# Kernel optimization log

Measured on AMD Instinct MI355X. Metric: run time of the kernel, lower is better.

The kernel has to match this reference:

```python
import jax, jax.numpy as jnp
import numpy as np

NUM_TAGS = 16
PAD_ID, START_ID, STOP_ID = 0, 14, 15
NEG = -10000.0
B, T, K = 1024, 512, NUM_TAGS


def setup_inputs() -> dict:
    key = jax.random.key(0)
    kh, kt, ky, kl = jax.random.split(key, 4)
    # transition matrix trans[to, from], with constraints from crf.__init__
    trans = jax.random.normal(kt, (K, K), jnp.float32)
    trans = (trans.at[START_ID, :].set(NEG)
                  .at[:, STOP_ID].set(NEG)
                  .at[:, PAD_ID].set(NEG)
                  .at[PAD_ID, :].set(NEG)
                  .at[PAD_ID, STOP_ID].set(0.0)
                  .at[PAD_ID, PAD_ID].set(0.0))
    # variable-length prefix mask (gt(0) on token ids in the original)
    lengths = jax.random.randint(kl, (B,), 1, T + 1)
    mask = (jnp.arange(T)[None, :] < lengths[:, None]).astype(jnp.float32)
    # gold tags: real tags in 1..13 on valid positions, PAD elsewhere
    y = 1 + jax.random.randint(ky, (B, T), 0, 13)
    y = jnp.where(mask > 0, y, PAD_ID).astype(jnp.int64)
    # emissions (output of fc in Net.forward)
    h = jax.random.normal(kh, (B, T, K), jnp.float32)
    return {"h": h, "y": y, "mask": mask, "trans": trans}


def _crf_forward_score(h, mask, trans):
    # partition function via log-sum-exp recurrence (crf.forward)
    alpha0 = jnp.full((h.shape[0], K), NEG, h.dtype).at[:, START_ID].set(0.0)

    def step(alpha, xs):
        emit_t, mask_t = xs  # [B,K], [B]
        # score.unsqueeze(1) + emit.unsqueeze(2) + trans -> [B, new, prev]
        s = alpha[:, None, :] + emit_t[:, :, None] + trans[None, :, :]
        new = jax.nn.logsumexp(s, axis=-1)  # [B,K]
        m = mask_t[:, None]
        return new * m + alpha * (1.0 - m), None

    alpha, _ = jax.lax.scan(step, alpha0,
                            (jnp.swapaxes(h, 0, 1), jnp.swapaxes(mask, 0, 1)))
    return jax.nn.logsumexp(alpha + trans[STOP_ID][None, :], axis=-1)  # [B]


def _crf_gold_score(h, y, mask, trans):
    # score of the gold path (crf.score), vectorized over time
    start = jnp.full((h.shape[0], 1), START_ID, y.dtype)
    y_ext = jnp.concatenate([start, y], axis=1)  # [B, T+1]
    y_prev, y_next = y_ext[:, :-1], y_ext[:, 1:]
    emit = jnp.take_along_axis(h, y_next[:, :, None], axis=2)[..., 0]  # [B,T]
    tr = trans[y_next, y_prev]  # [B,T]
    score = jnp.sum((emit + tr) * mask, axis=1)
    lengths = jnp.sum(mask, axis=1).astype(jnp.int32)  # index into y_ext
    last_tag = jnp.take_along_axis(y_ext, lengths[:, None].astype(y_ext.dtype), axis=1)[:, 0]
    return score + trans[STOP_ID, last_tag]


def reference(h, y, mask, trans):
    # Net.forward after fc: h *= mask, then CRF NLL
    h = h * mask[:, :, None]
    fwd = _crf_forward_score(h, mask, trans)
    gold = _crf_gold_score(h, y, mask, trans)
    return jnp.mean(fwd - gold)
```

## Files before the change

kernel.cpp:

```cpp
#include <hip/hip_runtime.h>
#include <hip/hip_bf16.h>

#define K 16
#define Bn 1024
#define Tn 512
#define START_ID 14
#define STOP_ID 15
#define LN2 0.69314718055994530942f
#define NCH 4
#define CL 128

typedef float f32x4 __attribute__((ext_vector_type(4)));
typedef short s16x4 __attribute__((ext_vector_type(4)));

static __device__ __forceinline__ s16x4 pack_bf16x4(float a, float b, float c, float d) {
    __hip_bfloat162 lo = __float22bfloat162_rn(float2{a, b});
    __hip_bfloat162 hi = __float22bfloat162_rn(float2{c, d});
    union { __hip_bfloat162 h2[2]; s16x4 v; } u;
    u.h2[0] = lo; u.h2[1] = hi;
    return u.v;
}

static __device__ __forceinline__ f32x4 unpack_bf16x4(s16x4 p) {
    union { s16x4 v; unsigned u[2]; } u; u.v = p;
    f32x4 r;
    r[0] = __uint_as_float(u.u[0] << 16);
    r[1] = __uint_as_float(u.u[0] & 0xffff0000u);
    r[2] = __uint_as_float(u.u[1] << 16);
    r[3] = __uint_as_float(u.u[1] & 0xffff0000u);
    return r;
}

__global__ __launch_bounds__(256) void crf_pre_gold(
    const float* __restrict__ h, const int* __restrict__ y,
    const float* __restrict__ trans,
    short* __restrict__ pe, float* __restrict__ gpart)
{
    int idx = blockIdx.x * 256 + threadIdx.x;
    const float* hp = h + (size_t)idx * K;
    f32x4 h0 = *(const f32x4*)(hp);
    f32x4 h1 = *(const f32x4*)(hp + 4);
    f32x4 h2 = *(const f32x4*)(hp + 8);
    f32x4 h3 = *(const f32x4*)(hp + 12);
    s16x4* pp = (s16x4*)(pe + (size_t)idx * K);
    pp[0] = pack_bf16x4(__expf(h0[0]), __expf(h0[1]), __expf(h0[2]), __expf(h0[3]));
    pp[1] = pack_bf16x4(__expf(h1[0]), __expf(h1[1]), __expf(h1[2]), __expf(h1[3]));
    pp[2] = pack_bf16x4(__expf(h2[0]), __expf(h2[1]), __expf(h2[2]), __expf(h2[3]));
    pp[3] = pack_bf16x4(__expf(h3[0]), __expf(h3[1]), __expf(h3[2]), __expf(h3[3]));

    int t = idx & (Tn - 1);
    int yt = y[idx];
    float g = 0.f;
    if (yt != 0) {
        int yp = (t == 0) ? START_ID : y[idx - 1];
        g = hp[yt] + trans[yt * K + yp];
        bool last = (t == Tn - 1) || (y[idx + 1] == 0);
        if (last) g += trans[STOP_ID * K + yt];
    }
#pragma unroll
    for (int off = 32; off; off >>= 1) g += __shfl_xor(g, off, 64);
    __shared__ float red[4];
    if ((threadIdx.x & 63) == 0) red[threadIdx.x >> 6] = g;
    __syncthreads();
    if (threadIdx.x == 0)
        gpart[blockIdx.x] = red[0] + red[1] + red[2] + red[3];
}

__global__ __launch_bounds__(256) void crf_chunk_combine(
    const short* __restrict__ pe, const int* __restrict__ y,
    const float* __restrict__ trans, float* __restrict__ fpart)
{
    __shared__ float Pl[NCH][16][17];
    __shared__ float El[NCH][16];

    int lane = threadIdx.x & 63;
    int c = threadIdx.x >> 6;
    int b = blockIdx.x;
    int s = lane & 15, q = lane >> 4;

    const int* yb = y + (size_t)b * Tn + c * CL;
    unsigned long long bal0 = __ballot(yb[lane] != 0);
    unsigned long long bal1 = __ballot(yb[64 + lane] != 0);
    int nv = __popcll(bal0) + __popcll(bal1);

    s16x4 afrag = pack_bf16x4(__expf(trans[s * K + 4 * q + 0]),
                              __expf(trans[s * K + 4 * q + 1]),
                              __expf(trans[s * K + 4 * q + 2]),
                              __expf(trans[s * K + 4 * q + 3]));

    f32x4 P;
    s16x4 bfrag;
#pragma unroll
    for (int r = 0; r < 4; ++r) {
        P[r] = (4 * q + r == s) ? 1.0f : 0.0f;
        ((short*)&bfrag)[r] = (4 * q + r == s) ? (short)0x3F80 : (short)0;
    }

    int esum = 0, pend = 0;
    const short* pb = pe + ((size_t)(b * Tn + c * CL)) * K + 4 * q;

    s16x4 cur[8], nxt[8];
#pragma unroll
    for (int r = 0; r < 8; ++r)
        cur[r] = *(const s16x4*)(pb + (size_t)r * K);

    for (int sb = 0; sb < CL / 8; ++sb) {
        int base = sb * 8;
        if (base >= nv) break;
        int n = nv - base; if (n > 8) n = 8;

        esum += pend;
        float sc = __uint_as_float((unsigned)(127 - pend) << 23);
        pend = 0;
        f32x4 pef[8];
#pragma unroll
        for (int r = 0; r < 8; ++r) pef[r] = unpack_bf16x4(cur[r]);
#pragma unroll
        for (int c2 = 0; c2 < 4; ++c2) pef[0][c2] *= sc;
#pragma unroll
        for (int r = 0; r < 8; ++r) {
            int tt = base + 8 + r; tt = tt > CL - 1 ? CL - 1 : tt;
            nxt[r] = *(const s16x4*)(pb + (size_t)tt * K);
        }
#pragma unroll
        for (int r = 0; r < 8; ++r) {
            if (r >= n) break;
            f32x4 C = __builtin_amdgcn_mfma_f32_16x16x16bf16_1k(
                afrag, bfrag, (f32x4){0.f, 0.f, 0.f, 0.f}, 0, 0, 0);
#pragma unroll
            for (int c2 = 0; c2 < 4; ++c2) C[c2] *= pef[r][c2];
            if (r == 5) {
                float m4 = fmaxf(fmaxf(C[0], C[1]), fmaxf(C[2], C[3]));
                m4 = fmaxf(m4, __shfl_xor(m4, 16, 64));
                m4 = fmaxf(m4, __shfl_xor(m4, 32, 64));
                int e = (int)(__float_as_uint(m4) >> 23) - 127;
                pend = e < -126 ? -126 : (e > 126 ? 126 : e);
            }
            bfrag = pack_bf16x4(C[0], C[1], C[2], C[3]);
            P = C;
        }
#pragma unroll
        for (int r = 0; r < 8; ++r) cur[r] = nxt[r];
    }

#pragma unroll
    for (int r = 0; r < 4; ++r)
        Pl[c][4 * q + r][s] = P[r];
    if (q == 0) El[c][s] = (float)esum;
    __syncthreads();

    if (c == 0) {
        int j = s;
        f32x4 Prow[NCH], Er[NCH];
#pragma unroll
        for (int cc = 0; cc < NCH; ++cc) {
#pragma unroll
            for (int r = 0; r < 4; ++r) {
                Prow[cc][r] = Pl[cc][j][4 * q + r];
                Er[cc][r]   = El[cc][4 * q + r];
            }
        }
        float Estop[4];
#pragma unroll
        for (int r = 0; r < 4; ++r)
            Estop[r] = __expf(trans[STOP_ID * K + 4 * q + r]);

        float ap[4];
#pragma unroll
        for (int r = 0; r < 4; ++r) ap[r] = (4 * q + r == START_ID) ? 1.0f : 0.0f;
        float ls = 0.f;

#pragma unroll
        for (int cc = 0; cc < NCH; ++cc) {
            float me = fmaxf(fmaxf(Er[cc][0], Er[cc][1]), fmaxf(Er[cc][2], Er[cc][3]));
            me = fmaxf(me, __shfl_xor(me, 16, 64));
            me = fmaxf(me, __shfl_xor(me, 32, 64));
            float w0 = ldexpf(ap[0], (int)(Er[cc][0] - me));
            float w1 = ldexpf(ap[1], (int)(Er[cc][1] - me));
            float w2 = ldexpf(ap[2], (int)(Er[cc][2] - me));
            float w3 = ldexpf(ap[3], (int)(Er[cc][3] - me));
            float acc = Prow[cc][0]*w0 + Prow[cc][1]*w1
                      + Prow[cc][2]*w2 + Prow[cc][3]*w3;
            acc += __shfl_xor(acc, 16, 64);
            acc += __shfl_xor(acc, 32, 64);
            float mj = acc;
#pragma unroll
            for (int off = 1; off < 16; off <<= 1)
                mj = fmaxf(mj, __shfl_xor(mj, off, 64));
            ls += me * LN2 + __logf(mj);
            float an = acc * (1.0f / mj);
#pragma unroll
            for (int r = 0; r < 4; ++r)
                ap[r] = __shfl(an, q * 4 + r, 16);
        }

        float part = ap[0]*Estop[0] + ap[1]*Estop[1]
                   + ap[2]*Estop[2] + ap[3]*Estop[3];
        part += __shfl_xor(part, 16, 64);
        part += __shfl_xor(part, 32, 64);
        if (lane == 0) fpart[b] = ls + __logf(part);
    }
}

__global__ __launch_bounds__(256) void crf_final(
    const float* __restrict__ fpart, const float* __restrict__ gpart,
    float* __restrict__ out)
{
    int t = threadIdx.x;
    float v = 0.f;
#pragma unroll
    for (int k2 = 0; k2 < 4; ++k2) v += fpart[t + 256 * k2];
#pragma unroll
    for (int k2 = 0; k2 < 8; ++k2) v -= gpart[t + 256 * k2];
#pragma unroll
    for (int off = 32; off; off >>= 1) v += __shfl_xor(v, off, 64);
    __shared__ float red[4];
    if ((t & 63) == 0) red[t >> 6] = v;
    __syncthreads();
    if (t == 0) out[0] = (red[0] + red[1] + red[2] + red[3]) * (1.0f / Bn);
}

extern "C" void kernel_launch(void* const* d_in, const int* in_sizes, int n_in,
                              void* d_out, int out_size, void* d_ws, size_t ws_size,
                              hipStream_t stream)
{
    const float* h     = (const float*)d_in[0];
    const int*   y     = (const int*)d_in[1];
    const float* trans = (const float*)d_in[3];
    float* out = (float*)d_out;

    float* gpart = (float*)d_ws;
    float* fpart = gpart + 2048;
    short* pe    = (short*)((float*)d_ws + 4096);

    crf_pre_gold<<<(Bn * Tn) / 256, 256, 0, stream>>>(h, y, trans, pe, gpart);
    crf_chunk_combine<<<Bn, 256, 0, stream>>>(pe, y, trans, fpart);
    crf_final<<<1, 256, 0, stream>>>(fpart, gpart, out);
}
```

Measured before the change: 107.8 us.

## Fuse emission exp and gold score into chunked MFMA CRF kernel

Removes the separate pre-pass kernel that wrote exp(h) as a bf16 buffer. The chunk kernel now reads raw h directly, one float per lane per timestep, and computes the exp inline. The emission factor is folded into the A operand (exp(h_t)*exp(trans)) rather than scaling the MFMA output, and the rescale factor is applied to P before packing. The gold-path score is computed per batch row inside the same kernel, which removes a kernel launch and the intermediate global round trip, at the cost of more exp and pack work on the serial dependency chain.

```diff
diff --git a/kernel.cpp b/kernel.cpp
--- a/kernel.cpp
+++ b/kernel.cpp
@@ -21,72 +21,56 @@
     return u.v;
 }
 
-static __device__ __forceinline__ f32x4 unpack_bf16x4(s16x4 p) {
-    union { s16x4 v; unsigned u[2]; } u; u.v = p;
-    f32x4 r;
-    r[0] = __uint_as_float(u.u[0] << 16);
-    r[1] = __uint_as_float(u.u[0] & 0xffff0000u);
-    r[2] = __uint_as_float(u.u[1] << 16);
-    r[3] = __uint_as_float(u.u[1] & 0xffff0000u);
-    return r;
-}
-
-__global__ __launch_bounds__(256) void crf_pre_gold(
+__global__ __launch_bounds__(256) void crf_all(
     const float* __restrict__ h, const int* __restrict__ y,
-    const float* __restrict__ trans,
-    short* __restrict__ pe, float* __restrict__ gpart)
-{
-    int idx = blockIdx.x * 256 + threadIdx.x;
-    const float* hp = h + (size_t)idx * K;
-    f32x4 h0 = *(const f32x4*)(hp);
-    f32x4 h1 = *(const f32x4*)(hp + 4);
-    f32x4 h2 = *(const f32x4*)(hp + 8);
-    f32x4 h3 = *(const f32x4*)(hp + 12);
-    s16x4* pp = (s16x4*)(pe + (size_t)idx * K);
-    pp[0] = pack_bf16x4(__expf(h0[0]), __expf(h0[1]), __expf(h0[2]), __expf(h0[3]));
-    pp[1] = pack_bf16x4(__expf(h1[0]), __expf(h1[1]), __expf(h1[2]), __expf(h1[3]));
-    pp[2] = pack_bf16x4(__expf(h2[0]), __expf(h2[1]), __expf(h2[2]), __expf(h2[3]));
-    pp[3] = pack_bf16x4(__expf(h3[0]), __expf(h3[1]), __expf(h3[2]), __expf(h3[3]));
-
-    int t = idx & (Tn - 1);
-    int yt = y[idx];
-    float g = 0.f;
-    if (yt != 0) {
-        int yp = (t == 0) ? START_ID : y[idx - 1];
-        g = hp[yt] + trans[yt * K + yp];
-        bool last = (t == Tn - 1) || (y[idx + 1] == 0);
-        if (last) g += trans[STOP_ID * K + yt];
-    }
-#pragma unroll
-    for (int off = 32; off; off >>= 1) g += __shfl_xor(g, off, 64);
-    __shared__ float red[4];
-    if ((threadIdx.x & 63) == 0) red[threadIdx.x >> 6] = g;
-    __syncthreads();
-    if (threadIdx.x == 0)
-        gpart[blockIdx.x] = red[0] + red[1] + red[2] + red[3];
-}
-
-__global__ __launch_bounds__(256) void crf_chunk_combine(
-    const short* __restrict__ pe, const int* __restrict__ y,
-    const float* __restrict__ trans, float* __restrict__ fpart)
+    const float* __restrict__ trans, float* __restrict__ res)
 {
     __shared__ float Pl[NCH][16][17];
     __shared__ float El[NCH][16];
+    __shared__ float Gl[NCH];
 
     int lane = threadIdx.x & 63;
     int c = threadIdx.x >> 6;
     int b = blockIdx.x;
     int s = lane & 15, q = lane >> 4;
 
-    const int* yb = y + (size_t)b * Tn + c * CL;
-    unsigned long long bal0 = __ballot(yb[lane] != 0);
-    unsigned long long bal1 = __ballot(yb[64 + lane] != 0);
+    const int* yseq = y + (size_t)b * Tn;
+    int y0 = yseq[c * CL + lane];
+    int y1 = yseq[c * CL + 64 + lane];
+    unsigned long long bal0 = __ballot(y0 != 0);
+    unsigned long long bal1 = __ballot(y1 != 0);
     int nv = __popcll(bal0) + __popcll(bal1);
 
-    s16x4 afrag = pack_bf16x4(__expf(trans[s * K + 4 * q + 0]),
-                              __expf(trans[s * K + 4 * q + 1]),
-                              __expf(trans[s * K + 4 * q + 2]),
-                              __expf(trans[s * K + 4 * q + 3]));
+    const float* hseq = h + ((size_t)b * Tn) * K;
+    float g = 0.f;
+    {
+        int t = c * CL + lane;
+        if (y0 != 0) {
+            int yp = (t == 0) ? START_ID : yseq[t - 1];
+            int tn = t + 1 > Tn - 1 ? Tn - 1 : t + 1;
+            float v = hseq[(size_t)t * K + y0] + trans[y0 * K + yp];
+            bool last = (t == Tn - 1) || (yseq[tn] == 0);
+            if (last) v += trans[STOP_ID * K + y0];
+            g += v;
+        }
+        int t2 = c * CL + 64 + lane;
+        if (y1 != 0) {
+            int yp = yseq[t2 - 1];
+            int tn = t2 + 1 > Tn - 1 ? Tn - 1 : t2 + 1;
+            float v = hseq[(size_t)t2 * K + y1] + trans[y1 * K + yp];
+            bool last = (t2 == Tn - 1) || (yseq[tn] == 0);
+            if (last) v += trans[STOP_ID * K + y1];
+            g += v;
+        }
+    }
+#pragma unroll
+    for (int off = 32; off; off >>= 1) g += __shfl_xor(g, off, 64);
+    if (lane == 0) Gl[c] = g;
+
+    float E0[4];
+#pragma unroll
+    for (int r = 0; r < 4; ++r)
+        E0[r] = __expf(trans[s * K + 4 * q + r]);
 
     f32x4 P;
     s16x4 bfrag;
@@ -97,12 +81,11 @@
     }
 
     int esum = 0, pend = 0;
-    const short* pb = pe + ((size_t)(b * Tn + c * CL)) * K + 4 * q;
-
-    s16x4 cur[8], nxt[8];
-#pragma unroll
-    for (int r = 0; r < 8; ++r)
-        cur[r] = *(const s16x4*)(pb + (size_t)r * K);
+    const float* hcs = hseq + (size_t)c * CL * K + s;
+
+    float hcur[8], hnxt[8];
+#pragma unroll
+    for (int r = 0; r < 8; ++r) hcur[r] = hcs[(size_t)r * K];
 
     for (int sb = 0; sb < CL / 8; ++sb) {
         int base = sb * 8;
@@ -112,23 +95,24 @@
         esum += pend;
         float sc = __uint_as_float((unsigned)(127 - pend) << 23);
         pend = 0;
-        f32x4 pef[8];
-#pragma unroll
-        for (int r = 0; r < 8; ++r) pef[r] = unpack_bf16x4(cur[r]);
-#pragma unroll
-        for (int c2 = 0; c2 < 4; ++c2) pef[0][c2] *= sc;
+        P[0] *= sc; P[1] *= sc; P[2] *= sc; P[3] *= sc;
+        bfrag = pack_bf16x4(P[0], P[1], P[2], P[3]);
+
+        float es[8];
+#pragma unroll
+        for (int r = 0; r < 8; ++r) es[r] = __expf(hcur[r]);
 #pragma unroll
         for (int r = 0; r < 8; ++r) {
             int tt = base + 8 + r; tt = tt > CL - 1 ? CL - 1 : tt;
-            nxt[r] = *(const s16x4*)(pb + (size_t)tt * K);
+            hnxt[r] = hcs[(size_t)tt * K];
         }
 #pragma unroll
         for (int r = 0; r < 8; ++r) {
             if (r >= n) break;
+            s16x4 afrag = pack_bf16x4(es[r] * E0[0], es[r] * E0[1],
+                                      es[r] * E0[2], es[r] * E0[3]);
             f32x4 C = __builtin_amdgcn_mfma_f32_16x16x16bf16_1k(
                 afrag, bfrag, (f32x4){0.f, 0.f, 0.f, 0.f}, 0, 0, 0);
-#pragma unroll
-            for (int c2 = 0; c2 < 4; ++c2) C[c2] *= pef[r][c2];
             if (r == 5) {
                 float m4 = fmaxf(fmaxf(C[0], C[1]), fmaxf(C[2], C[3]));
                 m4 = fmaxf(m4, __shfl_xor(m4, 16, 64));
@@ -140,7 +124,7 @@
             P = C;
         }
 #pragma unroll
-        for (int r = 0; r < 8; ++r) cur[r] = nxt[r];
+        for (int r = 0; r < 8; ++r) hcur[r] = hnxt[r];
     }
 
 #pragma unroll
@@ -198,20 +182,18 @@
                    + ap[2]*Estop[2] + ap[3]*Estop[3];
         part += __shfl_xor(part, 16, 64);
         part += __shfl_xor(part, 32, 64);
-        if (lane == 0) fpart[b] = ls + __logf(part);
+        if (lane == 0)
+            res[b] = ls + __logf(part) - (Gl[0] + Gl[1] + Gl[2] + Gl[3]);
     }
 }
 
 __global__ __launch_bounds__(256) void crf_final(
-    const float* __restrict__ fpart, const float* __restrict__ gpart,
-    float* __restrict__ out)
+    const float* __restrict__ res, float* __restrict__ out)
 {
     int t = threadIdx.x;
     float v = 0.f;
 #pragma unroll
-    for (int k2 = 0; k2 < 4; ++k2) v += fpart[t + 256 * k2];
-#pragma unroll
-    for (int k2 = 0; k2 < 8; ++k2) v -= gpart[t + 256 * k2];
+    for (int k2 = 0; k2 < 4; ++k2) v += res[t + 256 * k2];
 #pragma unroll
     for (int off = 32; off; off >>= 1) v += __shfl_xor(v, off, 64);
     __shared__ float red[4];
@@ -228,12 +210,8 @@
     const int*   y     = (const int*)d_in[1];
     const float* trans = (const float*)d_in[3];
     float* out = (float*)d_out;
-
-    float* gpart = (float*)d_ws;
-    float* fpart = gpart + 2048;
-    short* pe    = (short*)((float*)d_ws + 4096);
-
-    crf_pre_gold<<<(Bn * Tn) / 256, 256, 0, stream>>>(h, y, trans, pe, gpart);
-    crf_chunk_combine<<<Bn, 256, 0, stream>>>(pe, y, trans, fpart);
-    crf_final<<<1, 256, 0, stream>>>(fpart, gpart, out);
-}
+    float* res = (float*)d_ws;
+
+    crf_all<<<Bn, 256, 0, stream>>>(h, y, trans, res);
+    crf_final<<<1, 256, 0, stream>>>(res, out);
+}
```

New measurement: 106.7 us. No clear change (-1.0%).
